# Kernel tuning notes

Measured on AMD Instinct MI355X. Metric: run time of the kernel, lower is better.

## Reference

```python
import jax, jax.numpy as jnp
import numpy as np


def _linear(x, W, b):
    # torch nn.Linear: y = x @ W.T + b, W is [out, in]
    return x @ W.T + b


def _sage_layer(x, edge_index, Ws, bs, Wn, bn):
    # GraphSAGE: mean-aggregate neighbor features via scatter-add, then two linears.
    src, tgt = edge_index[0], edge_index[1]
    N = x.shape[0]
    agg = jax.ops.segment_sum(x[src], tgt, num_segments=N)            # [N, D]
    deg = jax.ops.segment_sum(jnp.ones(src.shape, x.dtype), tgt, num_segments=N)  # [N]
    neighbor_mean = agg / jnp.maximum(deg, 1.0)[:, None]
    return _linear(x, Ws, bs) + _linear(neighbor_mean, Wn, bn)


def setup_inputs() -> dict:
    key = jax.random.key(0)
    ks = jax.random.split(key, 16)
    N, ATTR, H, OUT, E = 50000, 125, 128, 128, 800000
    IN = ATTR + 3
    s = 0.05
    inp = {
        "attr_features": jax.random.normal(ks[0], (N, ATTR), jnp.float32),
        "clustering_coefficient": jax.random.uniform(ks[1], (N, 1), jnp.float32),
        "bidirectional_links_ratio": jax.random.uniform(ks[2], (N, 1), jnp.float32),
        "exist_nodes": jnp.ones((N,), jnp.float32),
        "W_in": s * jax.random.normal(ks[3], (H, IN), jnp.float32),
        "b_in": s * jax.random.normal(ks[4], (H,), jnp.float32),
        "W1_self": s * jax.random.normal(ks[5], (H, H), jnp.float32),
        "b1_self": s * jax.random.normal(ks[6], (H,), jnp.float32),
        "W1_neigh": s * jax.random.normal(ks[7], (H, H), jnp.float32),
        "b1_neigh": s * jax.random.normal(ks[8], (H,), jnp.float32),
        "W2_self": s * jax.random.normal(ks[9], (OUT, H), jnp.float32),
        "b2_self": s * jax.random.normal(ks[10], (OUT,), jnp.float32),
        "W2_neigh": s * jax.random.normal(ks[11], (OUT, H), jnp.float32),
        "b2_neigh": s * jax.random.normal(ks[12], (OUT,), jnp.float32),
        "edge_index": jax.random.randint(ks[13], (2, E), 0, N, jnp.int64),
    }
    return inp


def reference(attr_features, clustering_coefficient, bidirectional_links_ratio,
              exist_nodes, W_in, b_in, W1_self, b1_self, W1_neigh, b1_neigh,
              W2_self, b2_self, W2_neigh, b2_neigh, edge_index):
    exist_col = exist_nodes[:, None]                                   # [N, 1]
    x = jnp.concatenate(
        [attr_features, clustering_coefficient, bidirectional_links_ratio, exist_col],
        axis=1)                                                        # [N, attr_dim+3]
    x = jax.nn.relu(_linear(x, W_in, b_in))                            # dropout=0 -> identity
    x = _sage_layer(x, edge_index, W1_self, b1_self, W1_neigh, b1_neigh)
    x = jax.nn.relu(x)
    x = x * exist_col
    x = _sage_layer(x, edge_index, W2_self, b2_self, W2_neigh, b2_neigh)
    return x * exist_col
```

## Files before the change

kernel.cpp:

```cpp
#include <hip/hip_runtime.h>
#include <hip/hip_bf16.h>

typedef __attribute__((ext_vector_type(8))) short short8;
typedef __attribute__((ext_vector_type(4))) float floatx4;

__device__ inline unsigned short f2bf(float f) {
    unsigned u = __float_as_uint(f);
    u += 0x7fffu + ((u >> 16) & 1u);
    return (unsigned short)(u >> 16);
}


#define CHUNK_CAP 12288

__global__ void prep_weights(const float* __restrict__ w_in, const float* __restrict__ w1s,
                             const float* __restrict__ w1n, const float* __restrict__ w2s,
                             const float* __restrict__ w2n,
                             const float* __restrict__ b_in, const float* __restrict__ b1s,
                             const float* __restrict__ b1n, const float* __restrict__ b2s,
                             const float* __restrict__ b2n,
                             unsigned short* __restrict__ wb, float* __restrict__ biasf,
                             int* __restrict__ chunk_cursor) {
    int idx = blockIdx.x * 256 + threadIdx.x;
    if (idx < 5 * 16384) {
        int m = idx >> 14, j = idx & 16383;
        const float* src = (m == 0) ? w_in : (m == 1) ? w1s : (m == 2) ? w1n : (m == 3) ? w2s : w2n;
        wb[idx] = f2bf(src[j]);
    }
    if (idx < 128) {
        biasf[idx]       = b_in[idx];
        biasf[128 + idx] = b1s[idx] + b1n[idx];
        biasf[256 + idx] = b2s[idx] + b2n[idx];
    }
    if (blockIdx.x == 0 && threadIdx.x < 128)
        chunk_cursor[threadIdx.x] = threadIdx.x * CHUNK_CAP;
}

__global__ void build_x0(const float* __restrict__ attr, const float* __restrict__ cc,
                         const float* __restrict__ bl, const float* __restrict__ ex,
                         unsigned short* __restrict__ x0, int N, int ATTR) {
    int idx = blockIdx.x * 256 + threadIdx.x;
    if (idx >= N * 128) return;
    int row = idx >> 7, col = idx & 127;
    float v;
    if (col < ATTR)            v = attr[row * ATTR + col];
    else if (col == ATTR)      v = cc[row];
    else if (col == ATTR + 1)  v = bl[row];
    else                       v = ex[row];
    x0[idx] = f2bf(v);
}


#define BTILE 4096

__global__ __launch_bounds__(256) void bin_pass(const int* __restrict__ e,
                                                int* __restrict__ chunk_cursor,
                                                unsigned* __restrict__ packed_out,
                                                int E, int ntiles) {
    __shared__ unsigned buf[BTILE];
    __shared__ unsigned sbuf[BTILE];
    __shared__ int hist[128], offs[128], gbase[128], lcur[128];
    int t = threadIdx.x;
    for (int tile = blockIdx.x; tile < ntiles; tile += gridDim.x) {
        int e0 = tile * BTILE;
        int cnt = min(BTILE, E - e0);
        if (t < 128) hist[t] = 0;
        __syncthreads();
        for (int j = t; j < cnt; j += 256) {
            unsigned src = (unsigned)e[e0 + j];
            unsigned tgt = (unsigned)e[E + e0 + j];
            unsigned c = tgt >> 9;
            buf[j] = (c << 25) | (src << 9) | (tgt & 511u);
            atomicAdd(&hist[c], 1);
        }
        __syncthreads();
        if (t < 128) offs[t] = hist[t];
        __syncthreads();
        for (int o = 1; o < 128; o <<= 1) {
            int v = (t < 128 && t >= o) ? offs[t - o] : 0;
            __syncthreads();
            if (t < 128) offs[t] += v;
            __syncthreads();
        }
        if (t < 128) {
            int excl = offs[t] - hist[t];
            offs[t] = excl;
            lcur[t] = excl;
            gbase[t] = (hist[t] > 0) ? atomicAdd(&chunk_cursor[t], hist[t]) : 0;
        }
        __syncthreads();
        for (int j = t; j < cnt; j += 256) {
            unsigned v = buf[j];
            int c = v >> 25;
            int p = atomicAdd(&lcur[c], 1);
            sbuf[p] = v;
        }
        __syncthreads();
        int wv = t >> 6, lane = t & 63;
        for (int c = wv; c < 128; c += 4) {
            int n = hist[c], lo = offs[c], gb = gbase[c];
            for (int j = lane; j < n; j += 64)
                packed_out[gb + j] = sbuf[lo + j];
        }
        __syncthreads();
    }
}

__global__ __launch_bounds__(256) void chunk_csr(const unsigned* __restrict__ packed,
                                                 const int* __restrict__ chunk_cursor,
                                                 uint2* __restrict__ rows2,
                                                 int* __restrict__ colv, int N) {
    __shared__ int hist[512], offs[512], lcnt[512], pp[256];
    __shared__ int sbuf[CHUNK_CAP];
    int c = blockIdx.x;
    int base = c * CHUNK_CAP;
    int cnt = chunk_cursor[c] - base;
    int t = threadIdx.x;
    hist[t] = 0;
    hist[t + 256] = 0;
    __syncthreads();
    for (int j = t; j < cnt; j += 256)
        atomicAdd(&hist[packed[base + j] & 511u], 1);
    __syncthreads();
    int a0 = hist[2 * t], a1 = hist[2 * t + 1];
    pp[t] = a0 + a1;
    __syncthreads();
    for (int o = 1; o < 256; o <<= 1) {
        int v = (t >= o) ? pp[t - o] : 0;
        __syncthreads();
        pp[t] += v;
        __syncthreads();
    }
    int excl = pp[t] - (a0 + a1);
    offs[2 * t] = excl;
    offs[2 * t + 1] = excl + a0;
    lcnt[2 * t] = 0;
    lcnt[2 * t + 1] = 0;
    __syncthreads();
    for (int j = t; j < 512; j += 256) {
        int node = c * 512 + j;
        if (node < N) {
            uint2 r;
            r.x = base + offs[j];
            r.y = base + offs[j] + hist[j];
            rows2[node] = r;
        }
    }
    for (int j = t; j < cnt; j += 256) {
        unsigned v = packed[base + j];
        int node = v & 511u;
        int p = offs[node] + atomicAdd(&lcnt[node], 1);
        sbuf[p] = (v >> 9) & 0xFFFFu;
    }
    __syncthreads();
    for (int j = t; j < cnt; j += 256) colv[base + j] = sbuf[j];
}


__global__ __launch_bounds__(256) void agg_mean(const unsigned short* __restrict__ x,
                                                const uint2* __restrict__ rows2,
                                                const int* __restrict__ colv,
                                                unsigned short* __restrict__ nm, int N) {
    int wid = (blockIdx.x * 256 + threadIdx.x) >> 6;
    int lane = threadIdx.x & 63;
    if (wid >= N) return;
    uint2 r = rows2[wid];
    int s0 = r.x, s1 = r.y;
    int deg = s1 - s0;
    int mn = deg < 64 ? deg : 64;
    int cvec = (lane < mn) ? colv[s0 + lane] : 0;
    int quarter = lane >> 4;
    int cl = (lane & 15) * 8;
    float a0 = 0.f, a1 = 0.f, a2 = 0.f, a3 = 0.f;
    float a4 = 0.f, a5 = 0.f, a6 = 0.f, a7 = 0.f;
    int lim = mn - 1;
    for (int j = 0; j < mn; j += 32) {
        uint4 v[8];
        #pragma unroll
        for (int u = 0; u < 8; ++u) {
            int ei = j + 4 * u + quarter;
            int idx = (ei <= lim) ? ei : lim;
            int s = __shfl(cvec, idx, 64);
            v[u] = *(const uint4*)(x + (size_t)s * 128 + cl);
        }
        #pragma unroll
        for (int u = 0; u < 8; ++u) {
            int ei = j + 4 * u + quarter;
            if (ei <= lim) {
                a0 += __uint_as_float(v[u].x << 16);
                a1 += __uint_as_float(v[u].x & 0xffff0000u);
                a2 += __uint_as_float(v[u].y << 16);
                a3 += __uint_as_float(v[u].y & 0xffff0000u);
                a4 += __uint_as_float(v[u].z << 16);
                a5 += __uint_as_float(v[u].z & 0xffff0000u);
                a6 += __uint_as_float(v[u].w << 16);
                a7 += __uint_as_float(v[u].w & 0xffff0000u);
            }
        }
    }
    for (int e = s0 + 64; e < s1; e += 4) {
        int ei = e + quarter;
        int idx = (ei < s1) ? ei : s1 - 1;
        int s = colv[idx];
        uint4 v = *(const uint4*)(x + (size_t)s * 128 + cl);
        if (ei < s1) {
            a0 += __uint_as_float(v.x << 16);
            a1 += __uint_as_float(v.x & 0xffff0000u);
            a2 += __uint_as_float(v.y << 16);
            a3 += __uint_as_float(v.y & 0xffff0000u);
            a4 += __uint_as_float(v.z << 16);
            a5 += __uint_as_float(v.z & 0xffff0000u);
            a6 += __uint_as_float(v.w << 16);
            a7 += __uint_as_float(v.w & 0xffff0000u);
        }
    }
    a0 += __shfl_xor(a0, 16, 64); a0 += __shfl_xor(a0, 32, 64);
    a1 += __shfl_xor(a1, 16, 64); a1 += __shfl_xor(a1, 32, 64);
    a2 += __shfl_xor(a2, 16, 64); a2 += __shfl_xor(a2, 32, 64);
    a3 += __shfl_xor(a3, 16, 64); a3 += __shfl_xor(a3, 32, 64);
    a4 += __shfl_xor(a4, 16, 64); a4 += __shfl_xor(a4, 32, 64);
    a5 += __shfl_xor(a5, 16, 64); a5 += __shfl_xor(a5, 32, 64);
    a6 += __shfl_xor(a6, 16, 64); a6 += __shfl_xor(a6, 32, 64);
    a7 += __shfl_xor(a7, 16, 64); a7 += __shfl_xor(a7, 32, 64);
    if (quarter == 0) {
        float inv = 1.0f / (float)(deg > 1 ? deg : 1);
        a0 *= inv; a1 *= inv; a2 *= inv; a3 *= inv;
        a4 *= inv; a5 *= inv; a6 *= inv; a7 *= inv;
        uint4 o;
        o.x = ((unsigned)f2bf(a1) << 16) | (unsigned)f2bf(a0);
        o.y = ((unsigned)f2bf(a3) << 16) | (unsigned)f2bf(a2);
        o.z = ((unsigned)f2bf(a5) << 16) | (unsigned)f2bf(a4);
        o.w = ((unsigned)f2bf(a7) << 16) | (unsigned)f2bf(a6);
        *(uint4*)(nm + (size_t)wid * 128 + cl) = o;
    }
}


__global__ __launch_bounds__(256, 3) void gemm_fused(
    const unsigned short* __restrict__ X0, const unsigned short* __restrict__ X1,
    const unsigned short* __restrict__ W0, const unsigned short* __restrict__ W1,
    const float* __restrict__ bias, const float* __restrict__ ex,
    unsigned short* __restrict__ obf, float* __restrict__ of32,
    int N, int relu, int nphase) {
    __shared__ unsigned short lx[64 * 136];
    int tid = threadIdx.x;
    int lane = tid & 63;
    int w = tid >> 6;
    int node0 = blockIdx.x * 64;
    int n_off = w * 32;
    int q = lane >> 4;
    int m16 = lane & 15;

    short8 bf0[2][4], bf1[2][4];
    #pragma unroll
    for (int nt = 0; nt < 2; ++nt)
        #pragma unroll
        for (int kk = 0; kk < 4; ++kk)
            bf0[nt][kk] = *(const short8*)(W0 + (n_off + nt * 16 + m16) * 128 + kk * 32 + q * 8);
    if (nphase == 2) {
        #pragma unroll
        for (int nt = 0; nt < 2; ++nt)
            #pragma unroll
            for (int kk = 0; kk < 4; ++kk)
                bf1[nt][kk] = *(const short8*)(W1 + (n_off + nt * 16 + m16) * 128 + kk * 32 + q * 8);
    }

    floatx4 acc[4][2];
    for (int nt = 0; nt < 2; ++nt) {
        float bv = bias[n_off + nt * 16 + m16];
        floatx4 b4 = {bv, bv, bv, bv};
        for (int mt = 0; mt < 4; ++mt) acc[mt][nt] = b4;
    }

    for (int ph = 0; ph < nphase; ++ph) {
        const unsigned short* X = ph ? X1 : X0;
        for (int i = 0; i < 4; ++i) {
            int c = tid + 256 * i;
            int nd = c >> 4, ck = c & 15;
            short8 v = {0, 0, 0, 0, 0, 0, 0, 0};
            if (node0 + nd < N) v = *(const short8*)(X + (size_t)(node0 + nd) * 128 + ck * 8);
            *(short8*)(lx + nd * 136 + ck * 8) = v;
        }
        __syncthreads();
        for (int kk = 0; kk < 4; ++kk) {
            short8 a[4];
            for (int mt = 0; mt < 4; ++mt)
                a[mt] = *(const short8*)(lx + (mt * 16 + m16) * 136 + kk * 32 + q * 8);
            for (int mt = 0; mt < 4; ++mt) {
                const short8* b0 = ph ? &bf1[0][kk] : &bf0[0][kk];
                const short8* b1 = ph ? &bf1[1][kk] : &bf0[1][kk];
                acc[mt][0] = __builtin_amdgcn_mfma_f32_16x16x32_bf16(a[mt], *b0, acc[mt][0], 0, 0, 0);
                acc[mt][1] = __builtin_amdgcn_mfma_f32_16x16x32_bf16(a[mt], *b1, acc[mt][1], 0, 0, 0);
            }
        }
        __syncthreads();
    }

    for (int mt = 0; mt < 4; ++mt) {
        int rbase = node0 + mt * 16 + q * 4;
        for (int r = 0; r < 4; ++r) {
            int rr = rbase + r;
            if (rr >= N) continue;
            float e = ex ? ex[rr] : 1.0f;
            for (int nt = 0; nt < 2; ++nt) {
                float v = acc[mt][nt][r];
                if (relu) v = fmaxf(v, 0.0f);
                v *= e;
                int col = n_off + nt * 16 + m16;
                if (obf) obf[(size_t)rr * 128 + col] = f2bf(v);
                else     of32[(size_t)rr * 128 + col] = v;
            }
        }
    }
}


extern "C" void kernel_launch(void* const* d_in, const int* in_sizes, int n_in,
                              void* d_out, int out_size, void* d_ws, size_t ws_size,
                              hipStream_t stream) {
    const float* attr = (const float*)d_in[0];
    const float* cc   = (const float*)d_in[1];
    const float* bl   = (const float*)d_in[2];
    const float* ex   = (const float*)d_in[3];
    const float* w_in = (const float*)d_in[4];
    const float* b_in = (const float*)d_in[5];
    const float* w1s  = (const float*)d_in[6];
    const float* b1s  = (const float*)d_in[7];
    const float* w1n  = (const float*)d_in[8];
    const float* b1n  = (const float*)d_in[9];
    const float* w2s  = (const float*)d_in[10];
    const float* b2s  = (const float*)d_in[11];
    const float* w2n  = (const float*)d_in[12];
    const float* b2n  = (const float*)d_in[13];
    const int*   eidx = (const int*)d_in[14];

    int N = in_sizes[3];
    int ATTR = in_sizes[0] / N;
    int E = in_sizes[14] / 2;
    int Npad = ((N + 63) / 64) * 64;
    int nchunk = (N + 511) / 512;
    int ntilesE = (E + BTILE - 1) / BTILE;

    char* ws = (char*)d_ws;
    size_t off = 0;
    auto alloc = [&](size_t bytes) -> char* {
        off = (off + 255) & ~(size_t)255;
        char* p = ws + off;
        off += bytes;
        return p;
    };
    unsigned short* xa = (unsigned short*)alloc((size_t)Npad * 128 * 2);
    unsigned short* xb = (unsigned short*)alloc((size_t)Npad * 128 * 2);
    unsigned short* xc = (unsigned short*)alloc((size_t)Npad * 128 * 2);
    int* colv = (int*)alloc((size_t)128 * CHUNK_CAP * 4);
    unsigned* packed = (unsigned*)alloc((size_t)128 * CHUNK_CAP * 4);
    uint2* rows2 = (uint2*)alloc((size_t)N * 8);
    int* chunk_cursor = (int*)alloc(128 * 4);
    unsigned short* wb = (unsigned short*)alloc((size_t)5 * 16384 * 2);
    float* biasf = (float*)alloc(3 * 128 * 4);

    prep_weights<<<(5 * 16384 + 255) / 256, 256, 0, stream>>>(
        w_in, w1s, w1n, w2s, w2n, b_in, b1s, b1n, b2s, b2n, wb, biasf, chunk_cursor);
    build_x0<<<(N * 128 + 255) / 256, 256, 0, stream>>>(attr, cc, bl, ex, xa, N, ATTR);

    bin_pass<<<(ntilesE < 256 ? ntilesE : 256), 256, 0, stream>>>(eidx, chunk_cursor, packed, E, ntilesE);
    chunk_csr<<<nchunk, 256, 0, stream>>>(packed, chunk_cursor, rows2, colv, N);

    int gblk = Npad / 64;
    gemm_fused<<<gblk, 256, 0, stream>>>(xa, (const unsigned short*)nullptr,
                                         wb, (const unsigned short*)nullptr,
                                         biasf, (const float*)nullptr,
                                         xb, (float*)nullptr, N, 1, 1);
    agg_mean<<<(N + 3) / 4, 256, 0, stream>>>(xb, rows2, colv, xc, N);
    gemm_fused<<<gblk, 256, 0, stream>>>(xb, xc, wb + 16384, wb + 2 * 16384,
                                         biasf + 128, ex, xa, (float*)nullptr, N, 1, 2);
    agg_mean<<<(N + 3) / 4, 256, 0, stream>>>(xa, rows2, colv, xc, N);
    gemm_fused<<<gblk, 256, 0, stream>>>(xa, xc, wb + 3 * 16384, wb + 4 * 16384,
                                         biasf + 256, ex, (unsigned short*)nullptr,
                                         (float*)d_out, N, 0, 2);
}
```

Before: 246.6 us.

## Fuse input build, first GEMM and edge binning into one launch

Merges prep_weights, build_x0, the first linear layer and the edge-binning pass into a single kernel. Blocks are split by index: some bin edges while the rest build the bf16 input tile in LDS and run the input GEMM directly from the fp32 attributes. Weight conversion to bf16 and bias summation now happen inside each GEMM block, which removes the preprocessing launches and the intermediate x0 buffer at the cost of redundant per-block conversion. Binning now uses 256-node chunks with a smaller capacity, packs src<<16|tgt (so node ids must stay below 65536), and resets the cursor with a memset.

```diff
diff --git a/kernel.cpp b/kernel.cpp
--- a/kernel.cpp
+++ b/kernel.cpp
@@ -1,5 +1,4 @@
 #include <hip/hip_runtime.h>
-#include <hip/hip_bf16.h>
 
 typedef __attribute__((ext_vector_type(8))) short short8;
 typedef __attribute__((ext_vector_type(4))) float floatx4;
@@ -10,147 +9,184 @@
     return (unsigned short)(u >> 16);
 }
 
-
-#define CHUNK_CAP 12288
-
-__global__ void prep_weights(const float* __restrict__ w_in, const float* __restrict__ w1s,
-                             const float* __restrict__ w1n, const float* __restrict__ w2s,
-                             const float* __restrict__ w2n,
-                             const float* __restrict__ b_in, const float* __restrict__ b1s,
-                             const float* __restrict__ b1n, const float* __restrict__ b2s,
-                             const float* __restrict__ b2n,
-                             unsigned short* __restrict__ wb, float* __restrict__ biasf,
-                             int* __restrict__ chunk_cursor) {
-    int idx = blockIdx.x * 256 + threadIdx.x;
-    if (idx < 5 * 16384) {
-        int m = idx >> 14, j = idx & 16383;
-        const float* src = (m == 0) ? w_in : (m == 1) ? w1s : (m == 2) ? w1n : (m == 3) ? w2s : w2n;
-        wb[idx] = f2bf(src[j]);
-    }
-    if (idx < 128) {
-        biasf[idx]       = b_in[idx];
-        biasf[128 + idx] = b1s[idx] + b1n[idx];
-        biasf[256 + idx] = b2s[idx] + b2n[idx];
-    }
-    if (blockIdx.x == 0 && threadIdx.x < 128)
-        chunk_cursor[threadIdx.x] = threadIdx.x * CHUNK_CAP;
-}
-
-__global__ void build_x0(const float* __restrict__ attr, const float* __restrict__ cc,
-                         const float* __restrict__ bl, const float* __restrict__ ex,
-                         unsigned short* __restrict__ x0, int N, int ATTR) {
-    int idx = blockIdx.x * 256 + threadIdx.x;
-    if (idx >= N * 128) return;
-    int row = idx >> 7, col = idx & 127;
-    float v;
-    if (col < ATTR)            v = attr[row * ATTR + col];
-    else if (col == ATTR)      v = cc[row];
-    else if (col == ATTR + 1)  v = bl[row];
-    else                       v = ex[row];
-    x0[idx] = f2bf(v);
-}
-
-
+__device__ inline short8 pack8(const float4 a, const float4 b) {
+    short8 r;
+    r[0] = (short)f2bf(a.x); r[1] = (short)f2bf(a.y);
+    r[2] = (short)f2bf(a.z); r[3] = (short)f2bf(a.w);
+    r[4] = (short)f2bf(b.x); r[5] = (short)f2bf(b.y);
+    r[6] = (short)f2bf(b.z); r[7] = (short)f2bf(b.w);
+    return r;
+}
+
+#define CHUNK_CAP 6144
 #define BTILE 4096
 
-__global__ __launch_bounds__(256) void bin_pass(const int* __restrict__ e,
-                                                int* __restrict__ chunk_cursor,
-                                                unsigned* __restrict__ packed_out,
-                                                int E, int ntiles) {
-    __shared__ unsigned buf[BTILE];
-    __shared__ unsigned sbuf[BTILE];
-    __shared__ int hist[128], offs[128], gbase[128], lcur[128];
+
+__global__ __launch_bounds__(256, 3) void gemm0_bin(
+    const float* __restrict__ attr, const float* __restrict__ cc,
+    const float* __restrict__ bl, const float* __restrict__ ex,
+    const float* __restrict__ Wf, const float* __restrict__ bias,
+    unsigned short* __restrict__ out_bf,
+    const int* __restrict__ e, int* __restrict__ cursor,
+    unsigned* __restrict__ packed_out,
+    int N, int ATTR, int E, int nbin) {
+    __shared__ __align__(16) char smem[2 * BTILE * 4 + 4 * 256 * 4];
     int t = threadIdx.x;
-    for (int tile = blockIdx.x; tile < ntiles; tile += gridDim.x) {
-        int e0 = tile * BTILE;
+
+    if ((int)blockIdx.x < nbin) {
+        unsigned* buf  = (unsigned*)smem;
+        unsigned* sbuf = buf + BTILE;
+        int* hist  = (int*)(sbuf + BTILE);
+        int* offs  = hist + 256;
+        int* gbase = offs + 256;
+        int* lcur  = gbase + 256;
+        int e0 = blockIdx.x * BTILE;
         int cnt = min(BTILE, E - e0);
-        if (t < 128) hist[t] = 0;
+        hist[t] = 0;
         __syncthreads();
         for (int j = t; j < cnt; j += 256) {
             unsigned src = (unsigned)e[e0 + j];
             unsigned tgt = (unsigned)e[E + e0 + j];
-            unsigned c = tgt >> 9;
-            buf[j] = (c << 25) | (src << 9) | (tgt & 511u);
-            atomicAdd(&hist[c], 1);
-        }
-        __syncthreads();
-        if (t < 128) offs[t] = hist[t];
-        __syncthreads();
-        for (int o = 1; o < 128; o <<= 1) {
-            int v = (t < 128 && t >= o) ? offs[t - o] : 0;
+            buf[j] = (src << 16) | tgt;
+            atomicAdd(&hist[tgt >> 8], 1);
+        }
+        __syncthreads();
+        offs[t] = hist[t];
+        __syncthreads();
+        for (int o = 1; o < 256; o <<= 1) {
+            int v = (t >= o) ? offs[t - o] : 0;
             __syncthreads();
-            if (t < 128) offs[t] += v;
+            offs[t] += v;
             __syncthreads();
         }
-        if (t < 128) {
-            int excl = offs[t] - hist[t];
-            offs[t] = excl;
-            lcur[t] = excl;
-            gbase[t] = (hist[t] > 0) ? atomicAdd(&chunk_cursor[t], hist[t]) : 0;
-        }
+        int excl = offs[t] - hist[t];
+        offs[t] = excl;
+        lcur[t] = excl;
+        gbase[t] = (hist[t] > 0) ? t * CHUNK_CAP + atomicAdd(&cursor[t], hist[t]) : 0;
         __syncthreads();
         for (int j = t; j < cnt; j += 256) {
             unsigned v = buf[j];
-            int c = v >> 25;
+            int c = (v >> 8) & 0xFF;
             int p = atomicAdd(&lcur[c], 1);
             sbuf[p] = v;
         }
         __syncthreads();
         int wv = t >> 6, lane = t & 63;
-        for (int c = wv; c < 128; c += 4) {
+        for (int c = wv; c < 256; c += 4) {
             int n = hist[c], lo = offs[c], gb = gbase[c];
             for (int j = lane; j < n; j += 64)
                 packed_out[gb + j] = sbuf[lo + j];
         }
-        __syncthreads();
-    }
-}
+        return;
+    }
+
+    unsigned short* lx = (unsigned short*)smem;
+    int lane = t & 63;
+    int w = t >> 6;
+    int node0 = ((int)blockIdx.x - nbin) * 64;
+    int n_off = w * 32;
+    int q = lane >> 4;
+    int m16 = lane & 15;
+
+    short8 bf[2][4];
+    #pragma unroll
+    for (int nt = 0; nt < 2; ++nt)
+        #pragma unroll
+        for (int kk = 0; kk < 4; ++kk) {
+            const float* p = Wf + (n_off + nt * 16 + m16) * 128 + kk * 32 + q * 8;
+            bf[nt][kk] = pack8(*(const float4*)p, *(const float4*)(p + 4));
+        }
+
+    floatx4 acc[4][2];
+    #pragma unroll
+    for (int nt = 0; nt < 2; ++nt) {
+        float bv = bias[n_off + nt * 16 + m16];
+        floatx4 b4 = {bv, bv, bv, bv};
+        #pragma unroll
+        for (int mt = 0; mt < 4; ++mt) acc[mt][nt] = b4;
+    }
+
+    for (int i = 0; i < 32; ++i) {
+        int idx = t + 256 * i;
+        int nd = idx >> 7, col = idx & 127;
+        int row = node0 + nd;
+        float v = 0.0f;
+        if (row < N) {
+            if (col < ATTR)           v = attr[(size_t)row * ATTR + col];
+            else if (col == ATTR)     v = cc[row];
+            else if (col == ATTR + 1) v = bl[row];
+            else                      v = ex[row];
+        }
+        lx[nd * 136 + col] = f2bf(v);
+    }
+    __syncthreads();
+
+    #pragma unroll
+    for (int kk = 0; kk < 4; ++kk) {
+        short8 a[4];
+        #pragma unroll
+        for (int mt = 0; mt < 4; ++mt)
+            a[mt] = *(const short8*)(lx + (mt * 16 + m16) * 136 + kk * 32 + q * 8);
+        #pragma unroll
+        for (int mt = 0; mt < 4; ++mt) {
+            acc[mt][0] = __builtin_amdgcn_mfma_f32_16x16x32_bf16(a[mt], bf[0][kk], acc[mt][0], 0, 0, 0);
+            acc[mt][1] = __builtin_amdgcn_mfma_f32_16x16x32_bf16(a[mt], bf[1][kk], acc[mt][1], 0, 0, 0);
+        }
+    }
+
+    for (int mt = 0; mt < 4; ++mt) {
+        int rbase = node0 + mt * 16 + q * 4;
+        for (int r = 0; r < 4; ++r) {
+            int rr = rbase + r;
+            if (rr >= N) continue;
+            for (int nt = 0; nt < 2; ++nt) {
+                float v = fmaxf(acc[mt][nt][r], 0.0f);
+                out_bf[(size_t)rr * 128 + n_off + nt * 16 + m16] = f2bf(v);
+            }
+        }
+    }
+}
+
 
 __global__ __launch_bounds__(256) void chunk_csr(const unsigned* __restrict__ packed,
-                                                 const int* __restrict__ chunk_cursor,
+                                                 const int* __restrict__ cursor,
                                                  uint2* __restrict__ rows2,
                                                  int* __restrict__ colv, int N) {
-    __shared__ int hist[512], offs[512], lcnt[512], pp[256];
+    __shared__ int hist[256], offs[256], lcnt[256];
     __shared__ int sbuf[CHUNK_CAP];
     int c = blockIdx.x;
     int base = c * CHUNK_CAP;
-    int cnt = chunk_cursor[c] - base;
+    int cnt = cursor[c];
     int t = threadIdx.x;
     hist[t] = 0;
-    hist[t + 256] = 0;
     __syncthreads();
     for (int j = t; j < cnt; j += 256)
-        atomicAdd(&hist[packed[base + j] & 511u], 1);
-    __syncthreads();
-    int a0 = hist[2 * t], a1 = hist[2 * t + 1];
-    pp[t] = a0 + a1;
+        atomicAdd(&hist[packed[base + j] & 255u], 1);
+    __syncthreads();
+    offs[t] = hist[t];
     __syncthreads();
     for (int o = 1; o < 256; o <<= 1) {
-        int v = (t >= o) ? pp[t - o] : 0;
-        __syncthreads();
-        pp[t] += v;
-        __syncthreads();
-    }
-    int excl = pp[t] - (a0 + a1);
-    offs[2 * t] = excl;
-    offs[2 * t + 1] = excl + a0;
-    lcnt[2 * t] = 0;
-    lcnt[2 * t + 1] = 0;
-    __syncthreads();
-    for (int j = t; j < 512; j += 256) {
-        int node = c * 512 + j;
-        if (node < N) {
-            uint2 r;
-            r.x = base + offs[j];
-            r.y = base + offs[j] + hist[j];
-            rows2[node] = r;
-        }
+        int v = (t >= o) ? offs[t - o] : 0;
+        __syncthreads();
+        offs[t] += v;
+        __syncthreads();
+    }
+    int excl = offs[t] - hist[t];
+    offs[t] = excl;
+    lcnt[t] = 0;
+    __syncthreads();
+    int node = c * 256 + t;
+    if (node < N) {
+        uint2 r;
+        r.x = base + excl;
+        r.y = base + excl + hist[t];
+        rows2[node] = r;
     }
     for (int j = t; j < cnt; j += 256) {
         unsigned v = packed[base + j];
-        int node = v & 511u;
-        int p = offs[node] + atomicAdd(&lcnt[node], 1);
-        sbuf[p] = (v >> 9) & 0xFFFFu;
+        int nd = v & 255u;
+        int p = offs[nd] + atomicAdd(&lcnt[nd], 1);
+        sbuf[p] = v >> 16;
     }
     __syncthreads();
     for (int j = t; j < cnt; j += 256) colv[base + j] = sbuf[j];
@@ -238,10 +274,11 @@
 
 __global__ __launch_bounds__(256, 3) void gemm_fused(
     const unsigned short* __restrict__ X0, const unsigned short* __restrict__ X1,
-    const unsigned short* __restrict__ W0, const unsigned short* __restrict__ W1,
-    const float* __restrict__ bias, const float* __restrict__ ex,
+    const float* __restrict__ W0f, const float* __restrict__ W1f,
+    const float* __restrict__ b0, const float* __restrict__ b1,
+    const float* __restrict__ ex,
     unsigned short* __restrict__ obf, float* __restrict__ of32,
-    int N, int relu, int nphase) {
+    int N, int relu) {
     __shared__ unsigned short lx[64 * 136];
     int tid = threadIdx.x;
     int lane = tid & 63;
@@ -255,24 +292,24 @@
     #pragma unroll
     for (int nt = 0; nt < 2; ++nt)
         #pragma unroll
-        for (int kk = 0; kk < 4; ++kk)
-            bf0[nt][kk] = *(const short8*)(W0 + (n_off + nt * 16 + m16) * 128 + kk * 32 + q * 8);
-    if (nphase == 2) {
-        #pragma unroll
-        for (int nt = 0; nt < 2; ++nt)
-            #pragma unroll
-            for (int kk = 0; kk < 4; ++kk)
-                bf1[nt][kk] = *(const short8*)(W1 + (n_off + nt * 16 + m16) * 128 + kk * 32 + q * 8);
-    }
+        for (int kk = 0; kk < 4; ++kk) {
+            const float* p0 = W0f + (n_off + nt * 16 + m16) * 128 + kk * 32 + q * 8;
+            bf0[nt][kk] = pack8(*(const float4*)p0, *(const float4*)(p0 + 4));
+            const float* p1 = W1f + (n_off + nt * 16 + m16) * 128 + kk * 32 + q * 8;
+            bf1[nt][kk] = pack8(*(const float4*)p1, *(const float4*)(p1 + 4));
+        }
 
     floatx4 acc[4][2];
+    #pragma unroll
     for (int nt = 0; nt < 2; ++nt) {
-        float bv = bias[n_off + nt * 16 + m16];
+        int col = n_off + nt * 16 + m16;
+        float bv = b0[col] + b1[col];
         floatx4 b4 = {bv, bv, bv, bv};
+        #pragma unroll
         for (int mt = 0; mt < 4; ++mt) acc[mt][nt] = b4;
     }
 
-    for (int ph = 0; ph < nphase; ++ph) {
+    for (int ph = 0; ph < 2; ++ph) {
         const unsigned short* X = ph ? X1 : X0;
         for (int i = 0; i < 4; ++i) {
             int c = tid + 256 * i;
@@ -282,15 +319,18 @@
             *(short8*)(lx + nd * 136 + ck * 8) = v;
         }
         __syncthreads();
+        #pragma unroll
         for (int kk = 0; kk < 4; ++kk) {
             short8 a[4];
+            #pragma unroll
             for (int mt = 0; mt < 4; ++mt)
                 a[mt] = *(const short8*)(lx + (mt * 16 + m16) * 136 + kk * 32 + q * 8);
+            #pragma unroll
             for (int mt = 0; mt < 4; ++mt) {
-                const short8* b0 = ph ? &bf1[0][kk] : &bf0[0][kk];
-                const short8* b1 = ph ? &bf1[1][kk] : &bf0[1][kk];
-                acc[mt][0] = __builtin_amdgcn_mfma_f32_16x16x32_bf16(a[mt], *b0, acc[mt][0], 0, 0, 0);
-                acc[mt][1] = __builtin_amdgcn_mfma_f32_16x16x32_bf16(a[mt], *b1, acc[mt][1], 0, 0, 0);
+                const short8* p0 = ph ? &bf1[0][kk] : &bf0[0][kk];
+                const short8* p1 = ph ? &bf1[1][kk] : &bf0[1][kk];
+                acc[mt][0] = __builtin_amdgcn_mfma_f32_16x16x32_bf16(a[mt], *p0, acc[mt][0], 0, 0, 0);
+                acc[mt][1] = __builtin_amdgcn_mfma_f32_16x16x32_bf16(a[mt], *p1, acc[mt][1], 0, 0, 0);
             }
         }
         __syncthreads();
@@ -338,8 +378,9 @@
     int ATTR = in_sizes[0] / N;
     int E = in_sizes[14] / 2;
     int Npad = ((N + 63) / 64) * 64;
-    int nchunk = (N + 511) / 512;
+    int nchunk = (N + 255) / 256;
     int ntilesE = (E + BTILE - 1) / BTILE;
+    int gblk = Npad / 64;
 
     char* ws = (char*)d_ws;
     size_t off = 0;
@@ -349,33 +390,24 @@
         off += bytes;
         return p;
     };
-    unsigned short* xa = (unsigned short*)alloc((size_t)Npad * 128 * 2);
-    unsigned short* xb = (unsigned short*)alloc((size_t)Npad * 128 * 2);
-    unsigned short* xc = (unsigned short*)alloc((size_t)Npad * 128 * 2);
-    int* colv = (int*)alloc((size_t)128 * CHUNK_CAP * 4);
-    unsigned* packed = (unsigned*)alloc((size_t)128 * CHUNK_CAP * 4);
-    uint2* rows2 = (uint2*)alloc((size_t)N * 8);
-    int* chunk_cursor = (int*)alloc(128 * 4);
-    unsigned short* wb = (unsigned short*)alloc((size_t)5 * 16384 * 2);
-    float* biasf = (float*)alloc(3 * 128 * 4);
-
-    prep_weights<<<(5 * 16384 + 255) / 256, 256, 0, stream>>>(
-        w_in, w1s, w1n, w2s, w2n, b_in, b1s, b1n, b2s, b2n, wb, biasf, chunk_cursor);
-    build_x0<<<(N * 128 + 255) / 256, 256, 0, stream>>>(attr, cc, bl, ex, xa, N, ATTR);
-
-    bin_pass<<<(ntilesE < 256 ? ntilesE : 256), 256, 0, stream>>>(eidx, chunk_cursor, packed, E, ntilesE);
-    chunk_csr<<<nchunk, 256, 0, stream>>>(packed, chunk_cursor, rows2, colv, N);
-
-    int gblk = Npad / 64;
-    gemm_fused<<<gblk, 256, 0, stream>>>(xa, (const unsigned short*)nullptr,
-                                         wb, (const unsigned short*)nullptr,
-                                         biasf, (const float*)nullptr,
-                                         xb, (float*)nullptr, N, 1, 1);
-    agg_mean<<<(N + 3) / 4, 256, 0, stream>>>(xb, rows2, colv, xc, N);
-    gemm_fused<<<gblk, 256, 0, stream>>>(xb, xc, wb + 16384, wb + 2 * 16384,
-                                         biasf + 128, ex, xa, (float*)nullptr, N, 1, 2);
-    agg_mean<<<(N + 3) / 4, 256, 0, stream>>>(xa, rows2, colv, xc, N);
-    gemm_fused<<<gblk, 256, 0, stream>>>(xa, xc, wb + 3 * 16384, wb + 4 * 16384,
-                                         biasf + 256, ex, (unsigned short*)nullptr,
-                                         (float*)d_out, N, 0, 2);
-}
+    unsigned short* x1 = (unsigned short*)alloc((size_t)Npad * 128 * 2);
+    unsigned short* x2 = (unsigned short*)alloc((size_t)Npad * 128 * 2);
+    unsigned short* nm = (unsigned short*)alloc((size_t)Npad * 128 * 2);
+    int* colv        = (int*)alloc((size_t)nchunk * CHUNK_CAP * 4);
+    unsigned* packed = (unsigned*)alloc((size_t)nchunk * CHUNK_CAP * 4);
+    uint2* rows2     = (uint2*)alloc((size_t)N * 8);
+    int* cursor      = (int*)alloc(256 * 4);
+
+    hipMemsetAsync(cursor, 0, 256 * sizeof(int), stream);
+
+    gemm0_bin<<<ntilesE + gblk, 256, 0, stream>>>(attr, cc, bl, ex, w_in, b_in, x1,
+                                                  eidx, cursor, packed,
+                                                  N, ATTR, E, ntilesE);
+    chunk_csr<<<nchunk, 256, 0, stream>>>(packed, cursor, rows2, colv, N);
+    agg_mean<<<(N + 3) / 4, 256, 0, stream>>>(x1, rows2, colv, nm, N);
+    gemm_fused<<<gblk, 256, 0, stream>>>(x1, nm, w1s, w1n, b1s, b1n, ex,
+                                         x2, (float*)nullptr, N, 1);
+    agg_mean<<<(N + 3) / 4, 256, 0, stream>>>(x2, rows2, colv, nm, N);
+    gemm_fused<<<gblk, 256, 0, stream>>>(x2, nm, w2s, w2n, b2s, b2n, ex,
+                                         (unsigned short*)nullptr, (float*)d_out, N, 0);
+}
```

Result: slower. 264.4 us (+7.2%).
